# Performance work log

Hardware: AMD Instinct MI355X
Metric: run time of the kernel (lower is better)

The kernel has to match this reference:

```python
import jax, jax.numpy as jnp
import numpy as np
import math

DIM = 768
HEADS = 12
HEAD_DIM = DIM // HEADS
LENS_T = 64
LENS_S = 256
NTOK = LENS_T + LENS_S
BATCH = 32
MLP_HIDDEN = 4 * DIM
KEEP_RATIO = 0.7
LENS_KEEP = math.ceil(KEEP_RATIO * LENS_S)  # 180, static
NEG_INF = -1e9  # finite stand-in for masked_fill(-inf); mask is all-False here
LN_EPS = 1e-5


def layer_norm(x, g, b):
    m = jnp.mean(x, axis=-1, keepdims=True)
    v = jnp.var(x, axis=-1, keepdims=True)
    return (x - m) * jax.lax.rsqrt(v + LN_EPS) * g + b


def attention(x_normed, w_qkv, w_proj, b_proj, mask):
    # x_normed: [B,N,C]; torch: qkv Linear (no bias), split heads, softmax(qk*scale), proj
    B, N, C = x_normed.shape
    qkv = (x_normed @ w_qkv.T).reshape(B, N, 3, HEADS, HEAD_DIM)
    qkv = jnp.transpose(qkv, (2, 0, 3, 1, 4))  # [3,B,H,N,Dh]
    q, k, v = qkv[0], qkv[1], qkv[2]
    scores = jnp.einsum('bhqd,bhkd->bhqk', q, k) * (HEAD_DIM ** -0.5)
    scores = jnp.where(mask[:, None, None, :], NEG_INF, scores)
    attn = jax.nn.softmax(scores, axis=-1)  # [B,H,N,N]
    out = jnp.einsum('bhqk,bhkd->bhqd', attn, v)
    out = jnp.transpose(out, (0, 2, 1, 3)).reshape(B, N, C)
    return out @ w_proj.T + b_proj, attn


def mlp(x, w_fc1, b_fc1, w_fc2, b_fc2):
    h = jax.nn.gelu(x @ w_fc1.T + b_fc1, approximate=False)
    return h @ w_fc2.T + b_fc2


def candidate_topk(attn_all, tmpl_mask_f):
    # attn_all: [B,H,N,N]; template->search block, masked mean over template rows,
    # mean over heads, sort descending, split into keep/removed.
    attn_ts = attn_all[:, :, :LENS_T, LENS_T:]  # [B,H,T,S]
    w = tmpl_mask_f[:, None, :, None]  # [B,1,T,1]
    denom = jnp.sum(tmpl_mask_f, axis=1)[:, None, None]  # [B,1,1]
    scores = jnp.sum(attn_ts * w, axis=2) / denom  # [B,H,S] mean over kept template rows
    scores = jnp.mean(scores, axis=1)  # [B,S] mean over heads
    order = jnp.argsort(-scores, axis=1)  # descending
    return order[:, :LENS_KEEP], order[:, LENS_KEEP:]


def gather_tokens(tokens, topk_idx):
    tokens_t = tokens[:, :LENS_T]
    tokens_s = tokens[:, LENS_T:]
    kept = jnp.take_along_axis(tokens_s, topk_idx[:, :, None], axis=1)
    return jnp.concatenate([tokens_t, kept], axis=1)


def setup_inputs() -> dict:
    key = jax.random.key(0)
    ks = jax.random.split(key, 12)
    s = 0.02
    return {
        'x_rgb': jax.random.normal(ks[0], (BATCH, NTOK, DIM), jnp.float32),
        'x_tir': jax.random.normal(ks[1], (BATCH, NTOK, DIM), jnp.float32),
        'global_index_t': jax.random.randint(ks[2], (BATCH, LENS_T), 0, 64).astype(jnp.int64),
        'global_index_s': jax.random.randint(ks[3], (BATCH, LENS_S), 0, 256).astype(jnp.int64),
        'mask': jnp.zeros((BATCH, NTOK), dtype=bool),
        'cte_template_mask': jnp.ones((BATCH, LENS_T), dtype=bool),
        'keep_ratio_search': 0,
        'js_loss': jax.random.normal(ks[4], (1,), jnp.float32),
        'g1': jnp.ones((DIM,), jnp.float32),
        'b1': jnp.zeros((DIM,), jnp.float32),
        'w_qkv': jax.random.normal(ks[5], (3 * DIM, DIM), jnp.float32) * s,
        'w_proj': jax.random.normal(ks[6], (DIM, DIM), jnp.float32) * s,
        'b_proj': jnp.zeros((DIM,), jnp.float32),
        'g2': jnp.ones((DIM,), jnp.float32),
        'b2': jnp.zeros((DIM,), jnp.float32),
        'w_fc1': jax.random.normal(ks[7], (MLP_HIDDEN, DIM), jnp.float32) * s,
        'b_fc1': jnp.zeros((MLP_HIDDEN,), jnp.float32),
        'w_fc2': jax.random.normal(ks[8], (DIM, MLP_HIDDEN), jnp.float32) * s,
        'b_fc2': jnp.zeros((DIM,), jnp.float32),
    }


def reference(x_rgb, x_tir, global_index_t, global_index_s, mask, cte_template_mask,
              keep_ratio_search, js_loss, g1, b1, w_qkv, w_proj, b_proj, g2, b2,
              w_fc1, b_fc1, w_fc2, b_fc2):
    # dual-stream shared-weight attention
    rgb_attn_out, corrmap_rgb = attention(layer_norm(x_rgb, g1, b1), w_qkv, w_proj, b_proj, mask)
    tir_attn_out, corrmap_tir = attention(layer_norm(x_tir, g1, b1), w_qkv, w_proj, b_proj, mask)
    x_rgb = x_rgb + rgb_attn_out  # drop_path = Identity
    x_tir = x_tir + tir_attn_out

    # candidate elimination: both streams use the SAME fused attention map,
    # so the topk is identical for rgb and tir (torch calls it twice, same result)
    attn_all = corrmap_rgb + corrmap_tir
    tmpl_mask_f = cte_template_mask.astype(attn_all.dtype)
    topk_idx, non_topk_idx = candidate_topk(attn_all, tmpl_mask_f)
    x_rgb = gather_tokens(x_rgb, topk_idx)
    x_tir = gather_tokens(x_tir, topk_idx)
    global_index_s_new = jnp.take_along_axis(global_index_s, topk_idx, axis=1)
    removed_index_s = jnp.take_along_axis(global_index_s, non_topk_idx, axis=1)

    x_rgb = x_rgb + mlp(layer_norm(x_rgb, g2, b2), w_fc1, b_fc1, w_fc2, b_fc2)
    x_tir = x_tir + mlp(layer_norm(x_tir, g2, b2), w_fc1, b_fc1, w_fc2, b_fc2)
    return (x_rgb, x_tir, global_index_t, global_index_s_new, removed_index_s,
            corrmap_rgb, corrmap_tir, js_loss)
```

## Files before the change

### kernel.cpp

```cpp
#include <hip/hip_runtime.h>

typedef long long LL;
typedef unsigned short ushort_t;
typedef __attribute__((ext_vector_type(8))) short bfrag;
typedef __attribute__((ext_vector_type(8))) _Float16 hfrag;
typedef __attribute__((ext_vector_type(4))) float facc;
typedef __attribute__((ext_vector_type(4))) unsigned short us4;

constexpr int CDIM  = 768;
constexpr int HEADS = 12;
constexpr int LT    = 64;
constexpr int NTOK  = 320;
constexpr int BATCH = 32;
constexpr int LKEEP = 180;
constexpr int LREM  = 76;
constexpr int NK    = 244;

constexpr LL O_XRGB = 0;
constexpr LL O_XTIR = 5996544;
constexpr LL O_GIT  = 11993088;
constexpr LL O_GSN  = 11995136;
constexpr LL O_REM  = 12000896;
constexpr LL O_CR   = 12003328;
constexpr LL O_CT   = 51324928;
constexpr LL O_JS   = 90646528;

constexpr LL W_X1   = 0;
constexpr LL W_X1G  = 15728640;
constexpr LL W_SC   = 27721728;
constexpr LL W_ORD  = 27738112;
constexpr LL W_XN   = 27746304;
constexpr LL W_QKV  = 35610624;
constexpr LL W_ATT  = 59596800;

constexpr LL SZH = 7864320;

__device__ inline ushort_t cvt_bf16(float f) {
    union { float f; unsigned u; } x; x.f = f;
    unsigned u = x.u + 0x7fffu + ((x.u >> 16) & 1u);
    return (ushort_t)(u >> 16);
}
union h16u { _Float16 h; ushort_t u; };

#define GLL(gp, lp) __builtin_amdgcn_global_load_lds( \
    (const __attribute__((address_space(1))) unsigned int*)(gp), \
    (__attribute__((address_space(3))) unsigned int*)(lp), 16, 0, 0)

template<bool B16OUT>
__global__ __launch_bounds__(256)
void ln_kernel(const float* __restrict__ x, const float* __restrict__ g,
               const float* __restrict__ bta, void* __restrict__ y)
{
    LL row = blockIdx.x;
    const float* xr = x + row * 768;
    int t = threadIdx.x;
    float v0 = xr[t], v1 = xr[t + 256], v2 = xr[t + 512];
    __shared__ float red[256];
    red[t] = v0 + v1 + v2;
    __syncthreads();
    for (int s = 128; s; s >>= 1) { if (t < s) red[t] += red[t + s]; __syncthreads(); }
    float mean = red[0] / 768.0f;
    __syncthreads();
    float d0 = v0 - mean, d1 = v1 - mean, d2 = v2 - mean;
    red[t] = d0 * d0 + d1 * d1 + d2 * d2;
    __syncthreads();
    for (int s = 128; s; s >>= 1) { if (t < s) red[t] += red[t + s]; __syncthreads(); }
    float var = red[0] / 768.0f;
    float rs = 1.0f / sqrtf(var + 1e-5f);
    float o0 = d0 * rs * g[t]       + bta[t];
    float o1 = d1 * rs * g[t + 256] + bta[t + 256];
    float o2 = d2 * rs * g[t + 512] + bta[t + 512];
    if (B16OUT) {
        ushort_t* yr = (ushort_t*)y + row * 768;
        yr[t] = cvt_bf16(o0); yr[t + 256] = cvt_bf16(o1); yr[t + 512] = cvt_bf16(o2);
    } else {
        float* yr = (float*)y + row * 768;
        yr[t] = o0; yr[t + 256] = o1; yr[t + 512] = o2;
    }
}

__global__ __launch_bounds__(256)
void ln_f16x2(const float* __restrict__ x, const float* __restrict__ g,
              const float* __restrict__ bta,
              ushort_t* __restrict__ yh, ushort_t* __restrict__ yl)
{
    LL row = blockIdx.x;
    const float* xr = x + row * 768;
    int t = threadIdx.x;
    float v0 = xr[t], v1 = xr[t + 256], v2 = xr[t + 512];
    __shared__ float red[256];
    red[t] = v0 + v1 + v2;
    __syncthreads();
    for (int s = 128; s; s >>= 1) { if (t < s) red[t] += red[t + s]; __syncthreads(); }
    float mean = red[0] / 768.0f;
    __syncthreads();
    float d0 = v0 - mean, d1 = v1 - mean, d2 = v2 - mean;
    red[t] = d0 * d0 + d1 * d1 + d2 * d2;
    __syncthreads();
    for (int s = 128; s; s >>= 1) { if (t < s) red[t] += red[t + s]; __syncthreads(); }
    float var = red[0] / 768.0f;
    float rs = 1.0f / sqrtf(var + 1e-5f);
    #pragma unroll
    for (int c = 0; c < 3; ++c) {
        float d = (c == 0 ? d0 : c == 1 ? d1 : d2);
        int idx = t + c * 256;
        float o = d * rs * g[idx] + bta[idx];
        h16u hi, lo;
        hi.h = (_Float16)o;
        lo.h = (_Float16)(o - (float)hi.h);
        yh[row * 768 + idx] = hi.u;
        yl[row * 768 + idx] = lo.u;
    }
}

__global__ __launch_bounds__(256)
void cvt_f16x2(const float* __restrict__ in, ushort_t* __restrict__ oh,
               ushort_t* __restrict__ ol, int n)
{
    int i = (blockIdx.x * 256 + threadIdx.x) * 4;
    if (i >= n) return;
    float4 v = *(const float4*)(in + i);
    us4 h, l;
    #pragma unroll
    for (int j = 0; j < 4; ++j) {
        float f = (j == 0 ? v.x : j == 1 ? v.y : j == 2 ? v.z : v.w);
        h16u hh, ll;
        hh.h = (_Float16)f;
        ll.h = (_Float16)(f - (float)hh.h);
        h[j] = hh.u; l[j] = ll.u;
    }
    *(us4*)(oh + i) = h;
    *(us4*)(ol + i) = l;
}

__global__ __launch_bounds__(256)
void gemm_qkv(const ushort_t* __restrict__ Ah, const ushort_t* __restrict__ Al,
              const ushort_t* __restrict__ Bh, const ushort_t* __restrict__ Bl,
              ushort_t* __restrict__ Q1, ushort_t* __restrict__ Q2, ushort_t* __restrict__ Q3,
              ushort_t* __restrict__ K1, ushort_t* __restrict__ K2, ushort_t* __restrict__ K3,
              ushort_t* __restrict__ Vt)
{
    __shared__ ushort_t Ahs[4096], Als[4096], Bhs[4096], Bls[4096];
    const int t = threadIdx.x;
    const int wave = t >> 6, lane = t & 63;
    const int wr = wave >> 1, wc = wave & 1;
    const int lr = lane & 15, lh = lane >> 4;
    const LL bm = (LL)blockIdx.y * 128, bn = (LL)blockIdx.x * 128;
    const bool vt = (blockIdx.x >= 12);

    facc acc[4][4];
    #pragma unroll
    for (int i = 0; i < 4; ++i)
        #pragma unroll
        for (int j = 0; j < 4; ++j) acc[i][j] = (facc)(0.0f);

    const LL soff = (bm + wave * 16 + (lane >> 2)) * (LL)768 + (lane & 3) * 8;
    const LL boff = (bn + wave * 16 + (lane >> 2)) * (LL)768 + (lane & 3) * 8;
    const LL a64 = (LL)64 * 768;

    for (int k0 = 0; k0 < 768; k0 += 32) {
        __syncthreads();
        GLL(Ah + soff + k0,       &Ahs[wave * 512]);
        GLL(Ah + soff + k0 + a64, &Ahs[2048 + wave * 512]);
        GLL(Bh + boff + k0,       &Bhs[wave * 512]);
        GLL(Bh + boff + k0 + a64, &Bhs[2048 + wave * 512]);
        if (!vt) {
            GLL(Al + soff + k0,       &Als[wave * 512]);
            GLL(Al + soff + k0 + a64, &Als[2048 + wave * 512]);
            GLL(Bl + boff + k0,       &Bls[wave * 512]);
            GLL(Bl + boff + k0 + a64, &Bls[2048 + wave * 512]);
        }
        __syncthreads();
        hfrag ah[4], bh[4];
        #pragma unroll
        for (int mi = 0; mi < 4; ++mi)
            ah[mi] = *(const hfrag*)&Ahs[(wr * 64 + mi * 16 + lr) * 32 + lh * 8];
        #pragma unroll
        for (int ni = 0; ni < 4; ++ni)
            bh[ni] = *(const hfrag*)&Bhs[(wc * 64 + ni * 16 + lr) * 32 + lh * 8];
        if (!vt) {
            hfrag al[4], bl[4];
            #pragma unroll
            for (int mi = 0; mi < 4; ++mi)
                al[mi] = *(const hfrag*)&Als[(wr * 64 + mi * 16 + lr) * 32 + lh * 8];
            #pragma unroll
            for (int ni = 0; ni < 4; ++ni)
                bl[ni] = *(const hfrag*)&Bls[(wc * 64 + ni * 16 + lr) * 32 + lh * 8];
            #pragma unroll
            for (int mi = 0; mi < 4; ++mi)
                #pragma unroll
                for (int ni = 0; ni < 4; ++ni) {
                    acc[mi][ni] = __builtin_amdgcn_mfma_f32_16x16x32_f16(al[mi], bh[ni], acc[mi][ni], 0, 0, 0);
                    acc[mi][ni] = __builtin_amdgcn_mfma_f32_16x16x32_f16(ah[mi], bl[ni], acc[mi][ni], 0, 0, 0);
                    acc[mi][ni] = __builtin_amdgcn_mfma_f32_16x16x32_f16(ah[mi], bh[ni], acc[mi][ni], 0, 0, 0);
                }
        } else {
            #pragma unroll
            for (int mi = 0; mi < 4; ++mi)
                #pragma unroll
                for (int ni = 0; ni < 4; ++ni)
                    acc[mi][ni] = __builtin_amdgcn_mfma_f32_16x16x32_f16(ah[mi], bh[ni], acc[mi][ni], 0, 0, 0);
        }
    }

    #pragma unroll
    for (int mi = 0; mi < 4; ++mi)
        #pragma unroll
        for (int ni = 0; ni < 4; ++ni)
            #pragma unroll
            for (int j = 0; j < 4; ++j) {
                int r = (int)bm + wr * 64 + mi * 16 + lh * 4 + j;
                int c = (int)bn + wc * 64 + ni * 16 + lr;
                int b = r / 320, tt = r - b * 320;
                int s = c / 768, rem = c - s * 768;
                int h = rem >> 6, d = rem & 63;
                LL hb = (LL)(b * 12 + h) * 20480;
                float v = acc[mi][ni][j];
                if (s == 2) {
                    Vt[hb + d * 320 + tt] = cvt_bf16(v);
                } else {
                    h16u a1, a2, a3;
                    a1.h = (_Float16)v;
                    float rr = v - (float)a1.h;
                    a2.h = (_Float16)rr;
                    rr -= (float)a2.h;
                    a3.h = (_Float16)rr;
                    LL idx = hb + (LL)tt * 64 + d;
                    if (s == 0) { Q1[idx] = a1.u; Q2[idx] = a2.u; Q3[idx] = a3.u; }
                    else        { K1[idx] = a1.u; K2[idx] = a2.u; K3[idx] = a3.u; }
                }
            }
}

__global__ __launch_bounds__(256, 2)
void fused_attn(const ushort_t* __restrict__ Qh, const ushort_t* __restrict__ Qm,
                const ushort_t* __restrict__ Ql,
                const ushort_t* __restrict__ Kh, const ushort_t* __restrict__ Km,
                const ushort_t* __restrict__ Kl,
                const ushort_t* __restrict__ Vt,
                float* __restrict__ corr, ushort_t* __restrict__ attb,
                double* __restrict__ part, int mod)
{
    __shared__ __align__(128) unsigned char lds[81920];
    constexpr int PS = 40960;

    const int t = threadIdx.x;
    const int wave = t >> 6, lane = t & 63;
    const int lr = lane & 15, lh = lane >> 4;
    const int bh = blockIdx.y;
    const int b = bh / 12, h = bh - b * 12;
    const int r0 = blockIdx.x * 64;
    const LL kvbase = (LL)bh * 20480;

    const LL qoff = kvbase + (LL)(r0 + wave * 16 + lr) * 64 + lh * 8;
    hfrag qh0 = *(const hfrag*)(Qh + qoff), qh1 = *(const hfrag*)(Qh + qoff + 32);
    hfrag qm0 = *(const hfrag*)(Qm + qoff), qm1 = *(const hfrag*)(Qm + qoff + 32);
    hfrag ql0 = *(const hfrag*)(Ql + qoff), ql1 = *(const hfrag*)(Ql + qoff + 32);

    facc sacc[20];
    #pragma unroll
    for (int ct = 0; ct < 20; ++ct) sacc[ct] = (facc)(0.0f);

    #pragma unroll
    for (int ha = 0; ha < 5; ++ha) {
        if (ha) __syncthreads();
        #pragma unroll
        for (int i = 0; i < 6; ++i) {
            int id = wave * 6 + i;
            int s = id >> 3, c = id & 7;
            int local = c * 1024 + lane * 16;
            int row = local >> 7;
            int sb = local ^ ((row & 7) << 4);
            LL src = kvbase + (LL)ha * 4096 + (sb >> 1);
            const ushort_t* kp = (s == 0) ? Kh : (s == 1) ? Km : Kl;
            GLL(kp + src, &lds[s * 8192 + c * 1024]);
        }
        __syncthreads();

        #pragma unroll
        for (int ctl = 0; ctl < 4; ++ctl) {
            int tokl = ctl * 16 + lr;
            int x = (tokl & 7) << 4;
            const unsigned char* kb = lds + tokl * 128;
            int o0 = (lh * 16) ^ x;
            int o1 = (64 + lh * 16) ^ x;
            hfrag kh0 = *(const hfrag*)(kb + o0);
            hfrag kh1 = *(const hfrag*)(kb + o1);
            hfrag km0 = *(const hfrag*)(kb + 8192 + o0);
            hfrag km1 = *(const hfrag*)(kb + 8192 + o1);
            hfrag kl0 = *(const hfrag*)(kb + 16384 + o0);
            hfrag kl1 = *(const hfrag*)(kb + 16384 + o1);
            facc a = sacc[ha * 4 + ctl];
            a = __builtin_amdgcn_mfma_f32_16x16x32_f16(ql0, kh0, a, 0, 0, 0);
            a = __builtin_amdgcn_mfma_f32_16x16x32_f16(qh0, kl0, a, 0, 0, 0);
            a = __builtin_amdgcn_mfma_f32_16x16x32_f16(qm0, km0, a, 0, 0, 0);
            a = __builtin_amdgcn_mfma_f32_16x16x32_f16(qm0, kh0, a, 0, 0, 0);
            a = __builtin_amdgcn_mfma_f32_16x16x32_f16(qh0, km0, a, 0, 0, 0);
            a = __builtin_amdgcn_mfma_f32_16x16x32_f16(qh0, kh0, a, 0, 0, 0);
            a = __builtin_amdgcn_mfma_f32_16x16x32_f16(ql1, kh1, a, 0, 0, 0);
            a = __builtin_amdgcn_mfma_f32_16x16x32_f16(qh1, kl1, a, 0, 0, 0);
            a = __builtin_amdgcn_mfma_f32_16x16x32_f16(qm1, km1, a, 0, 0, 0);
            a = __builtin_amdgcn_mfma_f32_16x16x32_f16(qm1, kh1, a, 0, 0, 0);
            a = __builtin_amdgcn_mfma_f32_16x16x32_f16(qh1, km1, a, 0, 0, 0);
            a = __builtin_amdgcn_mfma_f32_16x16x32_f16(qh1, kh1, a, 0, 0, 0);
            sacc[ha * 4 + ctl] = a;
        }
    }

    __syncthreads();

    #pragma unroll
    for (int i = 0; i < 10; ++i) {
        int chunk = wave * 10 + i;
        int gs = chunk * 1024 + lane * 16;
        int d = gs / 640;
        int w = gs - d * 640;
        int sb = d * 640 + (w ^ ((d & 7) << 4));
        GLL(Vt + kvbase + (sb >> 1), &lds[chunk * 1024]);
    }

    float rs4[4];
    #pragma unroll
    for (int j = 0; j < 4; ++j) {
        float m = sacc[0][j];
        #pragma unroll
        for (int ct = 1; ct < 20; ++ct) m = fmaxf(m, sacc[ct][j]);
        #pragma unroll
        for (int o = 1; o < 16; o <<= 1) m = fmaxf(m, __shfl_xor(m, o, 64));
        m *= 0.125f;
        float s = 0.0f;
        #pragma unroll
        for (int ct = 0; ct < 20; ++ct) {
            float e = expf(sacc[ct][j] * 0.125f - m);
            sacc[ct][j] = e;
            s += e;
        }
        #pragma unroll
        for (int o = 1; o < 16; o <<= 1) s += __shfl_xor(s, o, 64);
        float rs = 1.0f / s;
        rs4[j] = rs;

        int prow = wave * 16 + lh * 4 + j;
        int xr = (prow & 7) << 4;
        #pragma unroll
        for (int ct = 0; ct < 20; ++ct) {
            int pcol = ct * 16 + lr;
            *(ushort_t*)(lds + PS + prow * 640 + ((pcol * 2) ^ xr)) =
                cvt_bf16(sacc[ct][j] * rs);
        }
    }

    __syncthreads();

    facc oacc[4];
    #pragma unroll
    for (int dt = 0; dt < 4; ++dt) oacc[dt] = (facc)(0.0f);
    int prow2 = wave * 16 + lr;
    int xp = (prow2 & 7) << 4;
    #pragma unroll
    for (int k0 = 0; k0 < 10; ++k0) {
        bfrag pa = *(const bfrag*)(lds + PS + prow2 * 640 + ((k0 * 64 + lh * 16) ^ xp));
        #pragma unroll
        for (int dt = 0; dt < 4; ++dt) {
            int dcol = dt * 16 + lr;
            bfrag vb = *(const bfrag*)(lds + dcol * 640 + ((k0 * 64 + lh * 16) ^ ((dcol & 7) << 4)));
            oacc[dt] = __builtin_amdgcn_mfma_f32_16x16x32_bf16(pa, vb, oacc[dt], 0, 0, 0);
        }
    }
    #pragma unroll
    for (int dt = 0; dt < 4; ++dt)
        #pragma unroll
        for (int j = 0; j < 4; ++j) {
            int grow = r0 + wave * 16 + lh * 4 + j;
            int gcol = h * 64 + dt * 16 + lr;
            attb[(LL)(b * 320 + grow) * 768 + gcol] = cvt_bf16(oacc[dt][j]);
        }

    __syncthreads();

    #pragma unroll
    for (int ct = 0; ct < 20; ++ct) {
        int pcol = ct * 16 + lr;
        #pragma unroll
        for (int j = 0; j < 4; ++j) {
            int prow = wave * 16 + lh * 4 + j;
            *(float*)(lds + (prow * 320 + pcol) * 4) = sacc[ct][j] * rs4[j];
        }
    }
    __syncthreads();

    float* crow = corr + (LL)bh * 102400 + (LL)r0 * 320;
    #pragma unroll
    for (int i = 0; i < 20; ++i) {
        int idx = i * 256 + t;
        int row = idx / 80, c4 = idx - row * 80;
        float4 v = *(const float4*)(lds + (row * 320 + c4 * 4) * 4);
        *(float4*)(crow + row * 320 + c4 * 4) = v;
    }

    if (blockIdx.x == 0) {
        double s64 = 0.0;
        for (int r = 0; r < 64; ++r)
            s64 += (double)*(const float*)(lds + (r * 320 + 64 + t) * 4);
        part[((LL)mod * 384 + bh) * 256 + t] = s64;
    }
}

template<int EPI>
__global__ __launch_bounds__(256)
void gemm_mfma(const ushort_t* __restrict__ A, const ushort_t* __restrict__ B,
               void* __restrict__ Cv, const float* __restrict__ bias,
               const float* __restrict__ res,
               int K, int lda, int ldb, int ldc, int ldres)
{
    __shared__ ushort_t As[4096];
    __shared__ ushort_t Bs[4096];
    const int t = threadIdx.x;
    const int wave = t >> 6, lane = t & 63;
    const int wr = wave >> 1, wc = wave & 1;
    const LL bm = (LL)blockIdx.y * 128, bn = (LL)blockIdx.x * 128;

    facc acc[4][4];
    #pragma unroll
    for (int i = 0; i < 4; ++i)
        #pragma unroll
        for (int j = 0; j < 4; ++j) acc[i][j] = (facc)(0.0f);

    const int lr = lane & 15, lh = lane >> 4;
    const ushort_t* gA = A + (bm + wave * 16 + (lane >> 2)) * lda + (lane & 3) * 8;
    const ushort_t* gB = B + (bn + wave * 16 + (lane >> 2)) * ldb + (lane & 3) * 8;
    const LL a64 = (LL)64 * lda, b64 = (LL)64 * ldb;

    for (int k0 = 0; k0 < K; k0 += 32) {
        __syncthreads();
        GLL(gA + k0,        &As[wave * 512]);
        GLL(gA + k0 + a64,  &As[2048 + wave * 512]);
        GLL(gB + k0,        &Bs[wave * 512]);
        GLL(gB + k0 + b64,  &Bs[2048 + wave * 512]);
        __syncthreads();
        bfrag a[4], b[4];
        #pragma unroll
        for (int m = 0; m < 4; ++m)
            a[m] = *(const bfrag*)&As[(wr * 64 + m * 16 + lr) * 32 + lh * 8];
        #pragma unroll
        for (int n = 0; n < 4; ++n)
            b[n] = *(const bfrag*)&Bs[(wc * 64 + n * 16 + lr) * 32 + lh * 8];
        #pragma unroll
        for (int m = 0; m < 4; ++m)
            #pragma unroll
            for (int n = 0; n < 4; ++n)
                acc[m][n] = __builtin_amdgcn_mfma_f32_16x16x32_bf16(a[m], b[n], acc[m][n], 0, 0, 0);
    }

    #pragma unroll
    for (int m = 0; m < 4; ++m) {
        #pragma unroll
        for (int n = 0; n < 4; ++n) {
            #pragma unroll
            for (int j = 0; j < 4; ++j) {
                LL r = bm + wr * 64 + m * 16 + lh * 4 + j;
                LL c = bn + wc * 64 + n * 16 + lr;
                float v = acc[m][n][j] + bias[c];
                if (EPI == 1) {
                    v = 0.5f * v * (erff(v * 0.70710678118654752f) + 1.0f);
                    ((ushort_t*)Cv)[r * ldc + c] = cvt_bf16(v);
                } else {
                    v += res[r * ldres + c];
                    ((float*)Cv)[r * ldc + c] = v;
                }
            }
        }
    }
}

__global__ __launch_bounds__(256)
void f32_to_bf16(const float* __restrict__ in, ushort_t* __restrict__ out, int n)
{
    int i = (blockIdx.x * 256 + threadIdx.x) * 4;
    if (i >= n) return;
    float4 v = *(const float4*)(in + i);
    us4 o;
    o[0] = cvt_bf16(v.x); o[1] = cvt_bf16(v.y);
    o[2] = cvt_bf16(v.z); o[3] = cvt_bf16(v.w);
    *(us4*)(out + i) = o;
}

__global__ __launch_bounds__(256)
void score_combine(const double* __restrict__ part, double* __restrict__ scores)
{
    int b = blockIdx.x, j = threadIdx.x;
    double acc = 0.0;
    for (int h = 0; h < 12; ++h) {
        LL i0 = ((LL)(b * 12 + h)) * 256 + j;
        acc += (part[i0] + part[98304 + i0]) / 64.0;
    }
    scores[b * 256 + j] = acc / 12.0;
}

__global__ __launch_bounds__(256)
void rank_kernel(const double* __restrict__ scores, const int* __restrict__ gis,
                 int* __restrict__ ord, float* __restrict__ onew, float* __restrict__ orem)
{
    int b = blockIdx.x, j = threadIdx.x;
    __shared__ double s[256];
    s[j] = scores[b * 256 + j];
    __syncthreads();
    double sj = s[j];
    int r = 0;
    for (int i = 0; i < 256; ++i) {
        double si = s[i];
        r += (si > sj) || (si == sj && i < j);
    }
    ord[b * 256 + r] = j;
    float gv = (float)gis[b * 256 + j];
    if (r < LKEEP) onew[b * LKEEP + r] = gv;
    else           orem[b * LREM + (r - LKEEP)] = gv;
}

__global__ void copy_misc(const int* __restrict__ git, const float* __restrict__ js,
                          float* __restrict__ out)
{
    int i = blockIdx.x * 256 + threadIdx.x;
    if (i < 2048)      out[O_GIT + i] = (float)git[i];
    else if (i == 2048) out[O_JS] = js[0];
}

__global__ __launch_bounds__(192)
void gather_kernel(const float* __restrict__ X1, const int* __restrict__ ord,
                   float* __restrict__ X1g)
{
    int rowid = blockIdx.x;
    int m   = rowid / (BATCH * NK);
    int rem = rowid - m * (BATCH * NK);
    int b   = rem / NK;
    int r   = rem - b * NK;
    int src = (r < LT) ? r : (LT + ord[b * 256 + (r - LT)]);
    const float4* s = (const float4*)(X1 + ((LL)m * BATCH * NTOK + b * NTOK + src) * 768);
    float4* d = (float4*)(X1g + (LL)rowid * 768);
    d[threadIdx.x] = s[threadIdx.x];
}

extern "C" void kernel_launch(void* const* d_in, const int* in_sizes, int n_in,
                              void* d_out, int out_size, void* d_ws, size_t ws_size,
                              hipStream_t stream)
{
    const float* xin_m[2] = { (const float*)d_in[0], (const float*)d_in[1] };
    const int*   git    = (const int*)d_in[2];
    const int*   gis    = (const int*)d_in[3];
    const float* js     = (const float*)d_in[7];
    const float* g1     = (const float*)d_in[8];
    const float* b1     = (const float*)d_in[9];
    const float* w_qkv  = (const float*)d_in[10];
    const float* w_proj = (const float*)d_in[11];
    const float* b_proj = (const float*)d_in[12];
    const float* g2     = (const float*)d_in[13];
    const float* b2     = (const float*)d_in[14];
    const float* w_fc1  = (const float*)d_in[15];
    const float* b_fc1  = (const float*)d_in[16];
    const float* w_fc2  = (const float*)d_in[17];
    const float* b_fc2  = (const float*)d_in[18];

    float* out = (float*)d_out;
    float* ws  = (float*)d_ws;

    double* sc  = (double*)(ws + W_SC);
    int*    ord = (int*)(ws + W_ORD);

    ushort_t* Xh  = (ushort_t*)(ws + W_XN);
    ushort_t* Xl  = Xh + SZH;
    ushort_t* ATTb = (ushort_t*)(ws + W_XN);
    ushort_t* QK  = (ushort_t*)(ws + W_QKV);
    ushort_t* Qh3 = QK,           *Qm3 = QK + SZH,     *Ql3 = QK + 2 * SZH;
    ushort_t* Kh3 = QK + 3 * SZH, *Km3 = QK + 4 * SZH, *Kl3 = QK + 5 * SZH;
    ushort_t* Wh  = (ushort_t*)(ws + W_ATT);
    ushort_t* Wl  = Wh + 1769472;
    ushort_t* Vt  = (ushort_t*)(ws + W_ATT + 2000000);
    double*   part = (double*)(ws + W_ATT + 6000000);
    ushort_t* WPROJb = (ushort_t*)(ws + W_X1G);
    ushort_t* WFC1b  = (ushort_t*)(ws + W_ATT);
    ushort_t* WFC2b  = (ushort_t*)(ws + W_ATT + 1179648);
    ushort_t* XN2b   = (ushort_t*)(ws + W_XN);
    ushort_t* H1b    = (ushort_t*)(ws + W_QKV);

    f32_to_bf16<<<dim3(576), dim3(256), 0, stream>>>(w_proj, WPROJb, 589824);
    cvt_f16x2<<<dim3(1728), dim3(256), 0, stream>>>(w_qkv, Wh, Wl, 1769472);

    for (int m = 0; m < 2; ++m) {
        const float* xin = xin_m[m];
        float* corr = out + (m ? O_CT : O_CR);
        float* X1m  = ws + W_X1 + (LL)m * BATCH * NTOK * CDIM;

        ln_f16x2<<<dim3(BATCH * NTOK), dim3(256), 0, stream>>>(xin, g1, b1, Xh, Xl);

        gemm_qkv<<<dim3(18, 80), dim3(256), 0, stream>>>(
            Xh, Xl, Wh, Wl, Qh3, Qm3, Ql3, Kh3, Km3, Kl3, Vt);

        fused_attn<<<dim3(5, BATCH * HEADS), dim3(256), 0, stream>>>(
            Qh3, Qm3, Ql3, Kh3, Km3, Kl3, Vt, corr, ATTb, part, m);

        gemm_mfma<2><<<dim3(6, 80), dim3(256), 0, stream>>>(
            ATTb, WPROJb, X1m, b_proj, xin, 768, 768, 768, 768, 768);
    }

    score_combine<<<dim3(BATCH), dim3(256), 0, stream>>>(part, sc);
    rank_kernel<<<dim3(BATCH), dim3(256), 0, stream>>>(sc, gis, ord,
                                                       out + O_GSN, out + O_REM);
    copy_misc<<<dim3(9), dim3(256), 0, stream>>>(git, js, out);
    gather_kernel<<<dim3(2 * BATCH * NK), dim3(192), 0, stream>>>(ws + W_X1, ord, ws + W_X1G);

    f32_to_bf16<<<dim3(2304), dim3(256), 0, stream>>>(w_fc1, WFC1b, 2359296);
    f32_to_bf16<<<dim3(2304), dim3(256), 0, stream>>>(w_fc2, WFC2b, 2359296);

    for (int m = 0; m < 2; ++m) {
        float* X1Gm = ws + W_X1G + (LL)m * BATCH * NK * CDIM;
        float* xout = out + (m ? O_XTIR : O_XRGB);

        ln_kernel<true><<<dim3(BATCH * NK), dim3(256), 0, stream>>>(X1Gm, g2, b2, XN2b);

        gemm_mfma<1><<<dim3(24, 61), dim3(256), 0, stream>>>(
            XN2b, WFC1b, H1b, b_fc1, nullptr, 768, 768, 768, 3072, 0);

        gemm_mfma<2><<<dim3(6, 61), dim3(256), 0, stream>>>(
            H1b, WFC2b, xout, b_fc2, X1Gm, 3072, 3072, 3072, 768, 768);
    }
}
```

Baseline: 1.040 ms.

## Double-buffer GEMM LDS tiles, XCD-remap attention grid, batch both MLP streams

The QKV and generic MFMA GEMMs now use double-buffered LDS tiles. The next k-slice's global-to-LDS load is issued before computing on the current one, leaving one barrier per iteration instead of two, so load latency can overlap compute. The fused attention kernel moves to a 1D grid that maps consecutive block IDs to the same (batch, head) within an XCD, aiming for better L2 reuse of K/V. The second-stage LayerNorm and MLP GEMMs for the RGB and TIR streams are merged into single launches over both streams' contiguous buffers, which cuts launch count and raises occupancy. In exchange, LDS per block doubles, which may lower occupancy, and the merged MLP relies on workspace regions being large enough for both streams.

```diff
diff --git a/kernel.cpp b/kernel.cpp
--- a/kernel.cpp
+++ b/kernel.cpp
@@ -140,7 +140,7 @@
               ushort_t* __restrict__ K1, ushort_t* __restrict__ K2, ushort_t* __restrict__ K3,
               ushort_t* __restrict__ Vt)
 {
-    __shared__ ushort_t Ahs[4096], Als[4096], Bhs[4096], Bls[4096];
+    __shared__ ushort_t Ahs[8192], Als[8192], Bhs[8192], Bls[8192];
     const int t = threadIdx.x;
     const int wave = t >> 6, lane = t & 63;
     const int wr = wave >> 1, wc = wave & 1;
@@ -158,34 +158,49 @@
     const LL boff = (bn + wave * 16 + (lane >> 2)) * (LL)768 + (lane & 3) * 8;
     const LL a64 = (LL)64 * 768;
 
+    GLL(Ah + soff,       &Ahs[wave * 512]);
+    GLL(Ah + soff + a64, &Ahs[2048 + wave * 512]);
+    GLL(Bh + boff,       &Bhs[wave * 512]);
+    GLL(Bh + boff + a64, &Bhs[2048 + wave * 512]);
+    if (!vt) {
+        GLL(Al + soff,       &Als[wave * 512]);
+        GLL(Al + soff + a64, &Als[2048 + wave * 512]);
+        GLL(Bl + boff,       &Bls[wave * 512]);
+        GLL(Bl + boff + a64, &Bls[2048 + wave * 512]);
+    }
+    __syncthreads();
+
+    int cur = 0;
     for (int k0 = 0; k0 < 768; k0 += 32) {
-        __syncthreads();
-        GLL(Ah + soff + k0,       &Ahs[wave * 512]);
-        GLL(Ah + soff + k0 + a64, &Ahs[2048 + wave * 512]);
-        GLL(Bh + boff + k0,       &Bhs[wave * 512]);
-        GLL(Bh + boff + k0 + a64, &Bhs[2048 + wave * 512]);
-        if (!vt) {
-            GLL(Al + soff + k0,       &Als[wave * 512]);
-            GLL(Al + soff + k0 + a64, &Als[2048 + wave * 512]);
-            GLL(Bl + boff + k0,       &Bls[wave * 512]);
-            GLL(Bl + boff + k0 + a64, &Bls[2048 + wave * 512]);
-        }
-        __syncthreads();
+        int nb = (cur ^ 1) * 4096;
+        if (k0 + 32 < 768) {
+            GLL(Ah + soff + k0 + 32,       &Ahs[nb + wave * 512]);
+            GLL(Ah + soff + k0 + 32 + a64, &Ahs[nb + 2048 + wave * 512]);
+            GLL(Bh + boff + k0 + 32,       &Bhs[nb + wave * 512]);
+            GLL(Bh + boff + k0 + 32 + a64, &Bhs[nb + 2048 + wave * 512]);
+            if (!vt) {
+                GLL(Al + soff + k0 + 32,       &Als[nb + wave * 512]);
+                GLL(Al + soff + k0 + 32 + a64, &Als[nb + 2048 + wave * 512]);
+                GLL(Bl + boff + k0 + 32,       &Bls[nb + wave * 512]);
+                GLL(Bl + boff + k0 + 32 + a64, &Bls[nb + 2048 + wave * 512]);
+            }
+        }
+        int cb = cur * 4096;
         hfrag ah[4], bh[4];
         #pragma unroll
         for (int mi = 0; mi < 4; ++mi)
-            ah[mi] = *(const hfrag*)&Ahs[(wr * 64 + mi * 16 + lr) * 32 + lh * 8];
+            ah[mi] = *(const hfrag*)&Ahs[cb + (wr * 64 + mi * 16 + lr) * 32 + lh * 8];
         #pragma unroll
         for (int ni = 0; ni < 4; ++ni)
-            bh[ni] = *(const hfrag*)&Bhs[(wc * 64 + ni * 16 + lr) * 32 + lh * 8];
+            bh[ni] = *(const hfrag*)&Bhs[cb + (wc * 64 + ni * 16 + lr) * 32 + lh * 8];
         if (!vt) {
             hfrag al[4], bl[4];
             #pragma unroll
             for (int mi = 0; mi < 4; ++mi)
-                al[mi] = *(const hfrag*)&Als[(wr * 64 + mi * 16 + lr) * 32 + lh * 8];
+                al[mi] = *(const hfrag*)&Als[cb + (wr * 64 + mi * 16 + lr) * 32 + lh * 8];
             #pragma unroll
             for (int ni = 0; ni < 4; ++ni)
-                bl[ni] = *(const hfrag*)&Bls[(wc * 64 + ni * 16 + lr) * 32 + lh * 8];
+                bl[ni] = *(const hfrag*)&Bls[cb + (wc * 64 + ni * 16 + lr) * 32 + lh * 8];
             #pragma unroll
             for (int mi = 0; mi < 4; ++mi)
                 #pragma unroll
@@ -201,6 +216,8 @@
                 for (int ni = 0; ni < 4; ++ni)
                     acc[mi][ni] = __builtin_amdgcn_mfma_f32_16x16x32_f16(ah[mi], bh[ni], acc[mi][ni], 0, 0, 0);
         }
+        __syncthreads();
+        cur ^= 1;
     }
 
     #pragma unroll
@@ -247,9 +264,14 @@
     const int t = threadIdx.x;
     const int wave = t >> 6, lane = t & 63;
     const int lr = lane & 15, lh = lane >> 4;
-    const int bh = blockIdx.y;
+    const int id  = blockIdx.x;
+    const int xcd = id & 7;
+    const int rem = id >> 3;
+    const int grp = rem / 5;
+    const int r0i = rem - grp * 5;
+    const int bh  = grp * 8 + xcd;
     const int b = bh / 12, h = bh - b * 12;
-    const int r0 = blockIdx.x * 64;
+    const int r0 = r0i * 64;
     const LL kvbase = (LL)bh * 20480;
 
     const LL qoff = kvbase + (LL)(r0 + wave * 16 + lr) * 64 + lh * 8;
@@ -266,8 +288,8 @@
         if (ha) __syncthreads();
         #pragma unroll
         for (int i = 0; i < 6; ++i) {
-            int id = wave * 6 + i;
-            int s = id >> 3, c = id & 7;
+            int id2 = wave * 6 + i;
+            int s = id2 >> 3, c = id2 & 7;
             int local = c * 1024 + lane * 16;
             int row = local >> 7;
             int sb = local ^ ((row & 7) << 4);
@@ -398,7 +420,7 @@
         *(float4*)(crow + row * 320 + c4 * 4) = v;
     }
 
-    if (blockIdx.x == 0) {
+    if (r0i == 0) {
         double s64 = 0.0;
         for (int r = 0; r < 64; ++r)
             s64 += (double)*(const float*)(lds + (r * 320 + 64 + t) * 4);
@@ -413,8 +435,8 @@
                const float* __restrict__ res,
                int K, int lda, int ldb, int ldc, int ldres)
 {
-    __shared__ ushort_t As[4096];
-    __shared__ ushort_t Bs[4096];
+    __shared__ ushort_t As[8192];
+    __shared__ ushort_t Bs[8192];
     const int t = threadIdx.x;
     const int wave = t >> 6, lane = t & 63;
     const int wr = wave >> 1, wc = wave & 1;
@@ -431,25 +453,36 @@
     const ushort_t* gB = B + (bn + wave * 16 + (lane >> 2)) * ldb + (lane & 3) * 8;
     const LL a64 = (LL)64 * lda, b64 = (LL)64 * ldb;
 
+    GLL(gA,        &As[wave * 512]);
+    GLL(gA + a64,  &As[2048 + wave * 512]);
+    GLL(gB,        &Bs[wave * 512]);
+    GLL(gB + b64,  &Bs[2048 + wave * 512]);
+    __syncthreads();
+
+    int cur = 0;
     for (int k0 = 0; k0 < K; k0 += 32) {
-        __syncthreads();
-        GLL(gA + k0,        &As[wave * 512]);
-        GLL(gA + k0 + a64,  &As[2048 + wave * 512]);
-        GLL(gB + k0,        &Bs[wave * 512]);
-        GLL(gB + k0 + b64,  &Bs[2048 + wave * 512]);
-        __syncthreads();
+        int nb = (cur ^ 1) * 4096;
+        if (k0 + 32 < K) {
+            GLL(gA + k0 + 32,        &As[nb + wave * 512]);
+            GLL(gA + k0 + 32 + a64,  &As[nb + 2048 + wave * 512]);
+            GLL(gB + k0 + 32,        &Bs[nb + wave * 512]);
+            GLL(gB + k0 + 32 + b64,  &Bs[nb + 2048 + wave * 512]);
+        }
+        int cb = cur * 4096;
         bfrag a[4], b[4];
         #pragma unroll
         for (int m = 0; m < 4; ++m)
-            a[m] = *(const bfrag*)&As[(wr * 64 + m * 16 + lr) * 32 + lh * 8];
+            a[m] = *(const bfrag*)&As[cb + (wr * 64 + m * 16 + lr) * 32 + lh * 8];
         #pragma unroll
         for (int n = 0; n < 4; ++n)
-            b[n] = *(const bfrag*)&Bs[(wc * 64 + n * 16 + lr) * 32 + lh * 8];
+            b[n] = *(const bfrag*)&Bs[cb + (wc * 64 + n * 16 + lr) * 32 + lh * 8];
         #pragma unroll
         for (int m = 0; m < 4; ++m)
             #pragma unroll
             for (int n = 0; n < 4; ++n)
                 acc[m][n] = __builtin_amdgcn_mfma_f32_16x16x32_bf16(a[m], b[n], acc[m][n], 0, 0, 0);
+        __syncthreads();
+        cur ^= 1;
     }
 
     #pragma unroll
@@ -595,7 +628,7 @@
         gemm_qkv<<<dim3(18, 80), dim3(256), 0, stream>>>(
             Xh, Xl, Wh, Wl, Qh3, Qm3, Ql3, Kh3, Km3, Kl3, Vt);
 
-        fused_attn<<<dim3(5, BATCH * HEADS), dim3(256), 0, stream>>>(
+        fused_attn<<<dim3(1920), dim3(256), 0, stream>>>(
             Qh3, Qm3, Ql3, Kh3, Km3, Kl3, Vt, corr, ATTb, part, m);
 
         gemm_mfma<2><<<dim3(6, 80), dim3(256), 0, stream>>>(
@@ -611,16 +644,12 @@
     f32_to_bf16<<<dim3(2304), dim3(256), 0, stream>>>(w_fc1, WFC1b, 2359296);
     f32_to_bf16<<<dim3(2304), dim3(256), 0, stream>>>(w_fc2, WFC2b, 2359296);
 
-    for (int m = 0; m < 2; ++m) {
-        float* X1Gm = ws + W_X1G + (LL)m * BATCH * NK * CDIM;
-        float* xout = out + (m ? O_XTIR : O_XRGB);
-
-        ln_kernel<true><<<dim3(BATCH * NK), dim3(256), 0, stream>>>(X1Gm, g2, b2, XN2b);
-
-        gemm_mfma<1><<<dim3(24, 61), dim3(256), 0, stream>>>(
-            XN2b, WFC1b, H1b, b_fc1, nullptr, 768, 768, 768, 3072, 0);
-
-        gemm_mfma<2><<<dim3(6, 61), dim3(256), 0, stream>>>(
-            H1b, WFC2b, xout, b_fc2, X1Gm, 3072, 3072, 3072, 768, 768);
-    }
-}
+    ln_kernel<true><<<dim3(2 * BATCH * NK), dim3(256), 0, stream>>>(
+        ws + W_X1G, g2, b2, XN2b);
+
+    gemm_mfma<1><<<dim3(24, 122), dim3(256), 0, stream>>>(
+        XN2b, WFC1b, H1b, b_fc1, nullptr, 768, 768, 768, 3072, 0);
+
+    gemm_mfma<2><<<dim3(6, 122), dim3(256), 0, stream>>>(
+        H1b, WFC2b, out + O_XRGB, b_fc2, ws + W_X1G, 3072, 3072, 3072, 768, 768);
+}
```

After: 983.3 us. 5.5% less time.
